# Optimization experiments

Measured on AMD Instinct MI355X. Metric: run time of the kernel, lower is better.

Reference implementation:

```python
import jax, jax.numpy as jnp
import numpy as np

N = 100000
E = 3200000
T = 8
F = 64


def _temporal_conv(x, src, dst, time_index, W, b):
    # time-bucketed segmented scatter-add: segment id = dst*T + t
    seg = dst * T + time_index                      # [E]
    msgs = x[src]                                   # [E, F] gather (x_j)
    agg = jax.ops.segment_sum(msgs, seg, num_segments=N * T)  # [N*T, F]
    cat = agg.reshape(N, T * x.shape[-1])           # concat over t blocks: [N, T*F]
    return jax.nn.relu(cat @ W + b)                 # temporal_lin + relu


def setup_inputs() -> dict:
    key = jax.random.key(0)
    ks = jax.random.split(key, 10)
    x = jax.random.normal(ks[0], (N, F), dtype=jnp.float32)
    edge_index = jax.random.randint(ks[1], (2, E), 0, N, dtype=jnp.int64)
    time_index = jax.random.randint(ks[2], (E,), 0, T, dtype=jnp.int64)
    s1 = 1.0 / np.sqrt(F * T)
    W1 = jax.random.uniform(ks[3], (F * T, 64), jnp.float32, -s1, s1)
    b1 = jax.random.uniform(ks[4], (64,), jnp.float32, -s1, s1)
    s2 = 1.0 / np.sqrt(64 * T)
    W2 = jax.random.uniform(ks[5], (64 * T, 64), jnp.float32, -s2, s2)
    b2 = jax.random.uniform(ks[6], (64,), jnp.float32, -s2, s2)
    s3 = 1.0 / np.sqrt(64)
    Wssl = jax.random.uniform(ks[7], (64, F), jnp.float32, -s3, s3)
    bssl = jax.random.uniform(ks[8], (F,), jnp.float32, -s3, s3)
    return {"x": x, "edge_index": edge_index, "time_index": time_index,
            "W1": W1, "b1": b1, "W2": W2, "b2": b2, "Wssl": Wssl, "bssl": bssl}


def reference(x, edge_index, time_index, W1, b1, W2, b2, Wssl, bssl):
    src, dst = edge_index[0], edge_index[1]  # flow source_to_target
    h = _temporal_conv(x, src, dst, time_index, W1, b1)
    h = jax.nn.relu(h)                        # outer relu in TemporalSSTGNN.forward
    h = _temporal_conv(h, src, dst, time_index, W2, b2)
    ssl = h @ Wssl + bssl                     # self_supervised_linear
    return (h, ssl)
```

## Files before the change

### kernel.cpp

```cpp
#include <hip/hip_runtime.h>
#include <hip/hip_bf16.h>

#define N_NODES 100000
#define N_EDGES 3200000
#define NB 391
#define NBP 400
#define CAP 9216
#define PCAP 20480
#define ZNODE N_NODES
#define NTILES 6250
#define AROW 520

typedef __attribute__((ext_vector_type(8))) short short8;
typedef __attribute__((ext_vector_type(4))) float floatx4;

__device__ __forceinline__ float bf2f(unsigned short u) {
    unsigned int x = ((unsigned int)u) << 16;
    return __builtin_bit_cast(float, x);
}
__device__ __forceinline__ unsigned short f2bf(float f) {
    unsigned int u = __builtin_bit_cast(unsigned int, f);
    unsigned int r = (u + 0x7FFFu + ((u >> 16) & 1u)) >> 16;
    return (unsigned short)r;
}


__global__ __launch_bounds__(512) void k_init(int* __restrict__ cursor) {
    int tid = threadIdx.x;
    if (tid < NB) cursor[tid] = tid * CAP;
}

__global__ __launch_bounds__(1024) void k_bscatter(const int* __restrict__ ei,
                                                   const int* __restrict__ ti,
                                                   int* __restrict__ cursor,
                                                   unsigned int* __restrict__ words) {
    __shared__ int h[NBP];
    __shared__ int bb[NBP];
    int tid = threadIdx.x;
    if (tid < NBP) h[tid] = 0;
    __syncthreads();
    int base = blockIdx.x * 4096;
    int breg[4], ofs[4];
    unsigned wreg[4];
#pragma unroll
    for (int i = 0; i < 4; ++i) {
        int e = base + i * 1024 + tid;
        bool v = e < N_EDGES;
        int dst = v ? ei[N_EDGES + e] : 0;
        int src = v ? ei[e] : 0;
        int tt  = v ? ti[e] : 0;
        int b = dst >> 8;
        breg[i] = v ? b : -1;
        wreg[i] = ((unsigned)src << 11) | ((unsigned)(dst & 255) << 3) | (unsigned)tt;
        ofs[i] = v ? atomicAdd(&h[b], 1) : 0;
    }
    __syncthreads();
    if (tid < NB) {
        int c = h[tid];
        bb[tid] = c ? atomicAdd(&cursor[tid], c) : 0;
    }
    __syncthreads();
#pragma unroll
    for (int i = 0; i < 4; ++i)
        if (breg[i] >= 0) words[bb[breg[i]] + ofs[i]] = wreg[i];
}

__global__ __launch_bounds__(1024) void k_lsort(const int* __restrict__ cursor,
                                                const unsigned int* __restrict__ words,
                                                int2* __restrict__ node_pm,
                                                int* __restrict__ gid_pad) {
    __shared__ int h[2048];
    __shared__ int ps[1024];
    __shared__ int nb[256];
    int tid = threadIdx.x;
    int b = blockIdx.x;
    int rb = b * CAP, re = cursor[b];
    h[tid] = 0; h[tid + 1024] = 0;
    __syncthreads();
    unsigned wreg[9];
    int ofs[9];
#pragma unroll
    for (int i = 0; i < 9; ++i) {
        int e = rb + i * 1024 + tid;
        bool v = e < re;
        unsigned w = v ? words[e] : 0u;
        wreg[i] = w;
        ofs[i] = v ? atomicAdd(&h[w & 2047u], 1) : -1;
    }
    __syncthreads();
    int sz = 0;
    if (tid < 256) {
        int m = 0;
#pragma unroll
        for (int t = 0; t < 8; ++t) { int c = h[tid * 8 + t]; m = c > m ? c : m; }
        m = (m + 1) & ~1;
        sz = m * 8;
    }
    ps[tid] = sz;
    __syncthreads();
    for (int off = 1; off < 1024; off <<= 1) {
        int t = (tid >= off) ? ps[tid - off] : 0;
        __syncthreads();
        ps[tid] += t;
        __syncthreads();
    }
    if (tid < 256) nb[tid] = ps[tid] - sz;
    __syncthreads();
    int bsz = ps[1023];
    int pbase = b * PCAP;
    for (int s = tid; s < bsz; s += 1024) gid_pad[pbase + s] = ZNODE;
    int gn = b * 256 + tid;
    if (tid < 256 && gn < N_NODES) node_pm[gn] = (int2){pbase + nb[tid], sz >> 3};
    __syncthreads();
#pragma unroll
    for (int i = 0; i < 9; ++i)
        if (ofs[i] >= 0) {
            unsigned w = wreg[i];
            int ls = (int)(w & 2047u);
            gid_pad[pbase + nb[ls >> 3] + ofs[i] * 8 + (ls & 7)] = (int)(w >> 11);
        }
}


__global__ void k_cvt(const float* __restrict__ x, unsigned short* __restrict__ xb,
                      unsigned short* __restrict__ h1b) {
    int i = blockIdx.x * 256 + threadIdx.x;
    if (i < N_NODES * 64) xb[i] = f2bf(x[i]);
    if (i < 64) {
        xb[(size_t)ZNODE * 64 + i] = 0;
        h1b[(size_t)ZNODE * 64 + i] = 0;
    }
}

__global__ void k_wprep(const float* __restrict__ W1, const float* __restrict__ W2,
                        const float* __restrict__ Wssl,
                        unsigned short* __restrict__ Wf1, unsigned short* __restrict__ Wf2,
                        unsigned short* __restrict__ Wsf) {
    int i = blockIdx.x * 256 + threadIdx.x;
    if (i < 512 * 64) {
        int k = i >> 6, o = i & 63;
        int c = o >> 4, m = o & 15;
        int ks = k >> 5, q = (k >> 3) & 3, j = k & 7;
        int pos = (((c * 16 + ks) * 64) + (m + 16 * q)) * 8 + j;
        Wf1[pos] = f2bf(W1[i]);
        Wf2[pos] = f2bf(W2[i]);
    }
    if (i < 64 * 64) {
        int k = i >> 6, o = i & 63;
        int c = o >> 4, m = o & 15;
        int ks = k >> 5, q = (k >> 3) & 3, j = k & 7;
        int pos = (((c * 2 + ks) * 64) + (m + 16 * q)) * 8 + j;
        Wsf[pos] = f2bf(Wssl[i]);
    }
}


__global__ __launch_bounds__(512) void k_fused(const int2* __restrict__ node_pm,
                                               const int* __restrict__ gid_pad,
                                               const unsigned short* __restrict__ xb,
                                               const unsigned short* __restrict__ Wf,
                                               const float* __restrict__ bias,
                                               unsigned short* __restrict__ out_bf,
                                               float* __restrict__ out_f32) {
    __shared__ __align__(16) unsigned short Atile[32 * AROW];
    int tid = threadIdx.x;
    int wave = tid >> 6, lane = tid & 63;
    int node_base = blockIdx.x * 32;
    int sel2 = lane >> 5, fp = lane & 31;
    int lofs = sel2 * 8;
    const unsigned int* xs32 = (const unsigned int*)xb;

    for (int i = 0; i < 4; ++i) {
        int nl = wave * 4 + i;
        int n = node_base + nl;
        int2 pm = node_pm[n];
        int pb = __builtin_amdgcn_readfirstlane(pm.x);
        int ml = __builtin_amdgcn_readfirstlane(pm.y);
        const int* gp = gid_pad + pb;
        float ax[8] = {0.f, 0.f, 0.f, 0.f, 0.f, 0.f, 0.f, 0.f};
        float ay[8] = {0.f, 0.f, 0.f, 0.f, 0.f, 0.f, 0.f, 0.f};
#pragma unroll 2
        for (int k = 0; k < ml; k += 2) {
            int kb = k * 8 + lofs;
            int ge[8];
#pragma unroll
            for (int t = 0; t < 8; ++t) ge[t] = gp[kb + t];
            unsigned pk[8];
#pragma unroll
            for (int t = 0; t < 8; ++t) pk[t] = xs32[((unsigned)ge[t] << 5) + fp];
#pragma unroll
            for (int t = 0; t < 8; ++t) {
                ax[t] += __builtin_bit_cast(float, pk[t] << 16);
                ay[t] += __builtin_bit_cast(float, pk[t] & 0xFFFF0000u);
            }
        }
#pragma unroll
        for (int t = 0; t < 8; ++t) {
            ax[t] += __shfl_xor(ax[t], 32, 64);
            ay[t] += __shfl_xor(ay[t], 32, 64);
        }
        if (lane < 32) {
            unsigned int* row = (unsigned int*)&Atile[nl * AROW];
#pragma unroll
            for (int t = 0; t < 8; ++t) {
                unsigned pkd = (unsigned)f2bf(ax[t]) | ((unsigned)f2bf(ay[t]) << 16);
                row[t * 32 + fp] = pkd;
            }
        }
    }
    __syncthreads();

    int nt = wave >> 2, c = wave & 3;
    int m = lane & 15, q = lane >> 4;
    floatx4 acc = (floatx4){0.f, 0.f, 0.f, 0.f};
    const short8* wf8 = (const short8*)Wf;
    const unsigned short* abase = &Atile[(nt * 16 + m) * AROW + q * 8];
#pragma unroll
    for (int ks = 0; ks < 16; ++ks) {
        short8 a = *(const short8*)(abase + ks * 32);
        short8 b = wf8[(c * 16 + ks) * 64 + lane];
        acc = __builtin_amdgcn_mfma_f32_16x16x32_bf16(a, b, acc, 0, 0, 0);
    }
    float bb = bias[c * 16 + m];
    int node0 = node_base + nt * 16;
#pragma unroll
    for (int i = 0; i < 4; ++i) {
        float v = acc[i] + bb;
        v = v > 0.f ? v : 0.f;
        int node = node0 + q * 4 + i;
        size_t idx = (size_t)node * 64 + c * 16 + m;
        if (out_bf)  out_bf[idx] = f2bf(v);
        if (out_f32) out_f32[idx] = v;
    }
}


__global__ __launch_bounds__(256) void k_sslm(const unsigned short* __restrict__ h2b,
                                              const unsigned short* __restrict__ Wsf,
                                              const float* __restrict__ bssl,
                                              float* __restrict__ out) {
    int wave = threadIdx.x >> 6, lane = threadIdx.x & 63;
    int tile = blockIdx.x * 4 + wave;
    if (tile >= NTILES) return;
    int m = lane & 15, q = lane >> 4;
    const unsigned short* arow = h2b + ((size_t)(tile * 16 + m)) * 64 + q * 8;
    floatx4 acc[4];
    for (int c = 0; c < 4; ++c) acc[c] = (floatx4){0.f, 0.f, 0.f, 0.f};
    const short8* wf8 = (const short8*)Wsf;
#pragma unroll
    for (int ks = 0; ks < 2; ++ks) {
        short8 a = *(const short8*)(arow + ks * 32);
#pragma unroll
        for (int c = 0; c < 4; ++c) {
            short8 b = wf8[(c * 2 + ks) * 64 + lane];
            acc[c] = __builtin_amdgcn_mfma_f32_16x16x32_bf16(a, b, acc[c], 0, 0, 0);
        }
    }
    int node0 = tile * 16;
#pragma unroll
    for (int c = 0; c < 4; ++c) {
        float bb = bssl[c * 16 + m];
#pragma unroll
        for (int i = 0; i < 4; ++i) {
            int node = node0 + q * 4 + i;
            out[(size_t)node * 64 + c * 16 + m] = acc[c][i] + bb;
        }
    }
}


extern "C" void kernel_launch(void* const* d_in, const int* in_sizes, int n_in,
                              void* d_out, int out_size, void* d_ws, size_t ws_size,
                              hipStream_t stream) {
    const float* x    = (const float*)d_in[0];
    const int*   ei   = (const int*)d_in[1];
    const int*   ti   = (const int*)d_in[2];
    const float* W1   = (const float*)d_in[3];
    const float* b1   = (const float*)d_in[4];
    const float* W2   = (const float*)d_in[5];
    const float* b2   = (const float*)d_in[6];
    const float* Wssl = (const float*)d_in[7];
    const float* bssl = (const float*)d_in[8];
    float* out = (float*)d_out;

    char* w = (char*)d_ws;
    auto alloc = [&](size_t bytes) -> char* {
        char* p = w;
        w += (bytes + 255) & ~(size_t)255;
        return p;
    };
    int* cursor   = (int*)alloc((size_t)NBP * 4);
    unsigned int* words = (unsigned int*)alloc((size_t)NB * CAP * 4);
    int2* node_pm = (int2*)alloc((size_t)N_NODES * 8);
    int* gid_pad  = (int*)alloc((size_t)NB * PCAP * 4);
    unsigned short* xb  = (unsigned short*)alloc((size_t)(N_NODES + 1) * 64 * 2);
    unsigned short* h1b = (unsigned short*)alloc((size_t)(N_NODES + 1) * 64 * 2);
    unsigned short* h2b = (unsigned short*)alloc((size_t)N_NODES * 64 * 2);
    unsigned short* Wf1 = (unsigned short*)alloc((size_t)512 * 64 * 2);
    unsigned short* Wf2 = (unsigned short*)alloc((size_t)512 * 64 * 2);
    unsigned short* Wsf = (unsigned short*)alloc((size_t)64 * 64 * 2);

    k_init<<<1, 512, 0, stream>>>(cursor);
    k_bscatter<<<(N_EDGES + 4095) / 4096, 1024, 0, stream>>>(ei, ti, cursor, words);
    k_lsort<<<NB, 1024, 0, stream>>>(cursor, words, node_pm, gid_pad);
    k_cvt<<<(N_NODES * 64 + 255) / 256, 256, 0, stream>>>(x, xb, h1b);
    k_wprep<<<(512 * 64 + 255) / 256, 256, 0, stream>>>(W1, W2, Wssl, Wf1, Wf2, Wsf);

    k_fused<<<N_NODES / 32, 512, 0, stream>>>(node_pm, gid_pad, xb, Wf1, b1, h1b, nullptr);
    k_fused<<<N_NODES / 32, 512, 0, stream>>>(node_pm, gid_pad, h1b, Wf2, b2, h2b, out);

    k_sslm<<<(NTILES + 3) / 4, 256, 0, stream>>>(h2b, Wsf, bssl, out + (size_t)N_NODES * 64);
}
```

Measured before the change: 348.4 us.

## Remap gather lanes to 16-byte loads per time bucket and pack with cvt_pk

Changes the gather lane mapping so each lane handles one time bucket and loads 8 bf16 features at once with a 16-byte vector load. The previous mapping used 4-byte loads covering all 8 buckets plus a cross-half shuffle reduction. This cuts the number of load instructions and removes the shuffle step. The accumulators are packed to bf16 with the hardware v_cvt_pk_bf16_f32 instruction and written as one 16-byte LDS store. There is less independent memory-level parallelism per lane, since only 2 loads are in flight per iteration instead of 8. The packing instruction's rounding may also differ slightly from the manual rounding routine.

```diff
diff --git a/kernel.cpp b/kernel.cpp
--- a/kernel.cpp
+++ b/kernel.cpp
@@ -166,9 +166,8 @@
     int tid = threadIdx.x;
     int wave = tid >> 6, lane = tid & 63;
     int node_base = blockIdx.x * 32;
-    int sel2 = lane >> 5, fp = lane & 31;
-    int lofs = sel2 * 8;
-    const unsigned int* xs32 = (const unsigned int*)xb;
+    int tl = lane >> 3, fo = lane & 7;
+    const uint4* xs = (const uint4*)xb;
 
     for (int i = 0; i < 4; ++i) {
         int nl = wave * 4 + i;
@@ -176,37 +175,38 @@
         int2 pm = node_pm[n];
         int pb = __builtin_amdgcn_readfirstlane(pm.x);
         int ml = __builtin_amdgcn_readfirstlane(pm.y);
-        const int* gp = gid_pad + pb;
-        float ax[8] = {0.f, 0.f, 0.f, 0.f, 0.f, 0.f, 0.f, 0.f};
-        float ay[8] = {0.f, 0.f, 0.f, 0.f, 0.f, 0.f, 0.f, 0.f};
-#pragma unroll 2
+        const int* gp = gid_pad + pb + tl;
+        float acc[8] = {0.f, 0.f, 0.f, 0.f, 0.f, 0.f, 0.f, 0.f};
         for (int k = 0; k < ml; k += 2) {
-            int kb = k * 8 + lofs;
-            int ge[8];
-#pragma unroll
-            for (int t = 0; t < 8; ++t) ge[t] = gp[kb + t];
-            unsigned pk[8];
-#pragma unroll
-            for (int t = 0; t < 8; ++t) pk[t] = xs32[((unsigned)ge[t] << 5) + fp];
-#pragma unroll
-            for (int t = 0; t < 8; ++t) {
-                ax[t] += __builtin_bit_cast(float, pk[t] << 16);
-                ay[t] += __builtin_bit_cast(float, pk[t] & 0xFFFF0000u);
-            }
+            int g0 = gp[k * 8];
+            int g1 = gp[k * 8 + 8];
+            uint4 p0 = xs[((unsigned)g0 << 3) + fo];
+            uint4 p1 = xs[((unsigned)g1 << 3) + fo];
+            acc[0] += __builtin_bit_cast(float, p0.x << 16);
+            acc[1] += __builtin_bit_cast(float, p0.x & 0xFFFF0000u);
+            acc[2] += __builtin_bit_cast(float, p0.y << 16);
+            acc[3] += __builtin_bit_cast(float, p0.y & 0xFFFF0000u);
+            acc[4] += __builtin_bit_cast(float, p0.z << 16);
+            acc[5] += __builtin_bit_cast(float, p0.z & 0xFFFF0000u);
+            acc[6] += __builtin_bit_cast(float, p0.w << 16);
+            acc[7] += __builtin_bit_cast(float, p0.w & 0xFFFF0000u);
+            acc[0] += __builtin_bit_cast(float, p1.x << 16);
+            acc[1] += __builtin_bit_cast(float, p1.x & 0xFFFF0000u);
+            acc[2] += __builtin_bit_cast(float, p1.y << 16);
+            acc[3] += __builtin_bit_cast(float, p1.y & 0xFFFF0000u);
+            acc[4] += __builtin_bit_cast(float, p1.z << 16);
+            acc[5] += __builtin_bit_cast(float, p1.z & 0xFFFF0000u);
+            acc[6] += __builtin_bit_cast(float, p1.w << 16);
+            acc[7] += __builtin_bit_cast(float, p1.w & 0xFFFF0000u);
         }
-#pragma unroll
-        for (int t = 0; t < 8; ++t) {
-            ax[t] += __shfl_xor(ax[t], 32, 64);
-            ay[t] += __shfl_xor(ay[t], 32, 64);
-        }
-        if (lane < 32) {
-            unsigned int* row = (unsigned int*)&Atile[nl * AROW];
-#pragma unroll
-            for (int t = 0; t < 8; ++t) {
-                unsigned pkd = (unsigned)f2bf(ax[t]) | ((unsigned)f2bf(ay[t]) << 16);
-                row[t * 32 + fp] = pkd;
-            }
-        }
+        unsigned r0, r1, r2, r3;
+        asm("v_cvt_pk_bf16_f32 %0, %1, %2" : "=v"(r0) : "v"(acc[0]), "v"(acc[1]));
+        asm("v_cvt_pk_bf16_f32 %0, %1, %2" : "=v"(r1) : "v"(acc[2]), "v"(acc[3]));
+        asm("v_cvt_pk_bf16_f32 %0, %1, %2" : "=v"(r2) : "v"(acc[4]), "v"(acc[5]));
+        asm("v_cvt_pk_bf16_f32 %0, %1, %2" : "=v"(r3) : "v"(acc[6]), "v"(acc[7]));
+        uint4 st;
+        st.x = r0; st.y = r1; st.z = r2; st.w = r3;
+        *(uint4*)(&Atile[nl * AROW + tl * 64 + fo * 8]) = st;
     }
     __syncthreads();
 
```

Result: faster. 339.9 us (-2.4%).
